# Performance work log

Hardware: AMD Instinct MI355X
Metric: run time of the kernel (lower is better)

## Reference

```python
import jax, jax.numpy as jnp
import numpy as np
from jax import lax

K = 3
STRIDE = 1
PAD = 1


def _active_sites(mask):
    # mask: [B, Cm, H, W] int. A patch is 'active' if ANY element of the
    # unfolded (im2col) patch is nonzero -> max-pool of (mask != 0) over the
    # same kernel/stride/padding window.
    m = jnp.any(mask != 0, axis=1, keepdims=True).astype(jnp.float32)  # [B,1,H,W]
    pooled = lax.reduce_window(
        m, 0.0, lax.max,
        window_dimensions=(1, 1, K, K),
        window_strides=(1, 1, STRIDE, STRIDE),
        padding=((0, 0), (0, 0), (PAD, PAD), (PAD, PAD)))
    return pooled > 0  # [B,1,H_out,W_out] bool


def reference(x, mask, weight, bias):
    # Faithful math of MyConv: conv2d(x, weight) + bias at active patch sites
    # (patches whose mask window contains any nonzero), exact zeros elsewhere.
    # masked_scatter in the original preserves patch order, so this equals
    # active * (conv + bias).
    conv = lax.conv_general_dilated(
        x, weight,
        window_strides=(STRIDE, STRIDE),
        padding=((PAD, PAD), (PAD, PAD)),
        dimension_numbers=('NCHW', 'OIHW', 'NCHW'))  # [B,C_out,H_out,W_out]
    active = _active_sites(mask)
    out = (conv + bias[None, :, None, None]) * active.astype(conv.dtype)
    return out


def setup_inputs() -> dict:
    key = jax.random.key(0)
    k1, k2, k3, k4 = jax.random.split(key, 4)
    B, C_in, C_out, H, W = 8, 128, 128, 128, 128
    x = jax.random.normal(k1, (B, C_in, H, W), dtype=jnp.float32)
    mask = jax.random.randint(k2, (B, 1, H, W), 0, 2, dtype=jnp.int32)
    fan_in = C_in * K * K
    bound = 1.0 / np.sqrt(fan_in)
    weight = jax.random.uniform(k3, (C_out, C_in, K, K), minval=-bound, maxval=bound, dtype=jnp.float32)
    bias = jax.random.uniform(k4, (C_out,), minval=-bound, maxval=bound, dtype=jnp.float32)
    return {"x": x, "mask": mask, "weight": weight, "bias": bias}
```

## Files before the change

kernel.cpp:

```cpp
#include <hip/hip_runtime.h>


typedef __bf16 bf16x8 __attribute__((ext_vector_type(8)));
typedef unsigned short u16x8 __attribute__((ext_vector_type(8)));
typedef float f32x4 __attribute__((ext_vector_type(4)));

__device__ __forceinline__ unsigned short f2bf(float f) {
    unsigned int u = __float_as_uint(f);
    u += 0x7fffu + ((u >> 16) & 1u);
    return (unsigned short)(u >> 16);
}

__global__ void setup_all(const float* __restrict__ x, const float* __restrict__ wgt,
                          unsigned short* __restrict__ xp, unsigned short* __restrict__ wpp) {
    __shared__ float Lf[32 * 132];
    const int t   = threadIdx.x;
    const int bid = blockIdx.x;

    if (bid >= 4160) {
        const int e    = (bid - 4160) * 256 + t;
        const int j    = e & 31;
        const int m    = (e >> 5) & 127;
        const int r    = e >> 12;
        const int kw   = r - (r / 3) * 3;
        const int cbkh = r / 3;
        const int cb   = cbkh & 3;
        const int kh   = cbkh >> 2;
        const int ci   = 4 * (j & 7) + (j >> 3);
        __builtin_nontemporal_store(f2bf(wgt[((m * 128 + cb * 32 + ci) * 3 + kh) * 3 + kw]), &wpp[e]);
        return;
    }

    const int hh2 = bid % 130;
    const int cb  = (bid / 130) & 3;
    const int b   = bid / 520;
    u16x8* slab = (u16x8*)(xp + (size_t)(((b * 4 + cb) * 130 + hh2)) * 4160);
    const u16x8 z = {0, 0, 0, 0, 0, 0, 0, 0};

    if (hh2 == 0 || hh2 == 129) {
        for (int k = t; k < 520; k += 256) __builtin_nontemporal_store(z, &slab[k]);
        return;
    }
    const int h = hh2 - 1;

    #pragma unroll
    for (int u = 0; u < 4; ++u) {
        const int f  = t + 256 * u;
        const int ci = f >> 5;
        const int w4 = f & 31;
        const f32x4 v = __builtin_nontemporal_load(
            (const f32x4*)(x + (((b * 128 + cb * 32 + ci) * 128 + h) << 7) + (w4 << 2)));
        *(f32x4*)&Lf[ci * 132 + (w4 << 2)] = v;
    }
    __syncthreads();

    for (int k = t; k < 520; k += 256) {
        const int r = k >> 2;
        const int c = k & 3;
        u16x8 o;
        if (r == 0 || r == 129) {
            o = z;
        } else {
            const int w  = r - 1;
            const int lc = c ^ ((r + (r >> 2)) & 3);
            #pragma unroll
            for (int s = 0; s < 8; ++s) o[s] = f2bf(Lf[(4 * s + lc) * 132 + w]);
        }
        __builtin_nontemporal_store(o, &slab[k]);
    }
}

__device__ __forceinline__ void stage_slabs(const unsigned char* gx, unsigned char* ls, int t) {
    const int g    = t >> 6;
    const int lane = t & 63;
    #pragma unroll
    for (int u = 0; u < 8; ++u)
        __builtin_amdgcn_global_load_lds(
            (const __attribute__((address_space(1))) unsigned int*)(gx + u * 2048 + g * 1024 + lane * 16),
            (__attribute__((address_space(3))) unsigned int*)(ls + u * 2048 + g * 1024),
            16, 0, 0);
    if (t < 16)
        __builtin_amdgcn_global_load_lds(
            (const __attribute__((address_space(1))) unsigned int*)(gx + 16384 + t * 16),
            (__attribute__((address_space(3))) unsigned int*)(ls + 16384),
            16, 0, 0);
}

__global__ __launch_bounds__(128, 2)
void myconv5(const unsigned short* __restrict__ xp,
             const int* __restrict__ mask,
             const unsigned short* __restrict__ wp,
             const float* __restrict__ bias,
             float* __restrict__ out)
{
    __shared__ __align__(16) unsigned char Xs[2][16640];
    __shared__ float act[256];

    const int t = threadIdx.x;
    const int b     = blockIdx.x & 7;
    const int r8    = blockIdx.x >> 3;
    const int mhalf = r8 & 1;
    const int h0    = (r8 >> 1) << 1;

    const int lane = t & 63;
    const int l16  = lane & 15;
    const int q    = lane >> 4;
    const int g    = t >> 6;

    const unsigned char* xpB = (const unsigned char*)xp;

    stage_slabs(xpB + (size_t)((b * 4 + 0) * 130 + h0 + 0) * 8320, &Xs[0][0], t);

    #pragma unroll
    for (int gg = 0; gg < 2; ++gg) {
        const int h = h0 + gg;
        int any = 0;
        #pragma unroll
        for (int kh = 0; kh < 3; ++kh) {
            int hh = h + kh - 1;
            if ((unsigned)hh < 128u) {
                const int* mrow = mask + (b * 128 + hh) * 128;
                #pragma unroll
                for (int kw = 0; kw < 3; ++kw) {
                    int ww = t + kw - 1;
                    if ((unsigned)ww < 128u) any |= mrow[ww];
                }
            }
        }
        act[gg * 128 + t] = any ? 1.0f : 0.0f;
    }

    int bb[3];
    #pragma unroll
    for (int kw = 0; kw < 3; ++kw) {
        const int rr   = l16 + kw;
        const int slot = q ^ ((rr + (rr >> 2)) & 3);
        bb[kw] = g * 8320 + rr * 64 + (slot << 4);
    }

    const unsigned char* agl = (const unsigned char*)wp + (mhalf * 64 + l16) * 64 + q * 16;

    f32x4 acc[4][8];
    const f32x4 fzero = {0.f, 0.f, 0.f, 0.f};
    #pragma unroll
    for (int i = 0; i < 4; ++i)
        #pragma unroll
        for (int j = 0; j < 8; ++j)
            acc[i][j] = fzero;

    __syncthreads();

    for (int r = 0; r < 12; ++r) {
        if (r < 11) {
            const int rn = r + 1;
            stage_slabs(xpB + (size_t)((b * 4 + (rn & 3)) * 130 + h0 + (rn >> 2)) * 8320,
                        &Xs[(rn & 1)][0], t);
        }

        const unsigned char* ar = agl + r * 24576;
        const unsigned char* xb = &Xs[r & 1][0];
        #pragma unroll
        for (int kw = 0; kw < 3; ++kw) {
            bf16x8 af[4];
            #pragma unroll
            for (int i = 0; i < 4; ++i)
                af[i] = *(const bf16x8*)(ar + kw * 8192 + i * 1024);
            bf16x8 bfr[8];
            #pragma unroll
            for (int j = 0; j < 8; ++j)
                bfr[j] = *(const bf16x8*)(xb + bb[kw] + j * 1024);
            #pragma unroll
            for (int i = 0; i < 4; ++i)
                #pragma unroll
                for (int j = 0; j < 8; ++j)
                    acc[i][j] = __builtin_amdgcn_mfma_f32_16x16x32_bf16(af[i], bfr[j], acc[i][j], 0, 0, 0);
        }

        __syncthreads();
    }

    #pragma unroll
    for (int i = 0; i < 4; ++i) {
        const int m0 = mhalf * 64 + (i << 4) + (q << 2);
        const f32x4 bv = *(const f32x4*)(bias + m0);
        #pragma unroll
        for (int j = 0; j < 8; ++j) {
            const int w = (j << 4) + l16;
            const float a = act[(g << 7) + w];
            float* base = out + (((b << 7) + m0) << 14) + ((h0 + g) << 7) + w;
            #pragma unroll
            for (int rg = 0; rg < 4; ++rg)
                base[rg << 14] = (acc[i][j][rg] + bv[rg]) * a;
        }
    }
}

#define LDAF 40
__global__ __launch_bounds__(256, 2)
void myconv_fb(const float* __restrict__ x,
               const int* __restrict__ mask,
               const float* __restrict__ wgt,
               const float* __restrict__ bias,
               float* __restrict__ out)
{
    __shared__ unsigned short As[128 * LDAF];
    __shared__ unsigned short Bs[128 * LDAF];
    __shared__ float act[128];

    const int t   = threadIdx.x;
    const int blk = blockIdx.x;
    const int b   = blk >> 7;
    const int h   = blk & 127;

    if (t < 128) {
        int any = 0;
        #pragma unroll
        for (int kh = 0; kh < 3; ++kh) {
            int hh = h + kh - 1;
            if ((unsigned)hh < 128u) {
                const int* mrow = mask + (b * 128 + hh) * 128;
                #pragma unroll
                for (int kw = 0; kw < 3; ++kw) {
                    int ww = t + kw - 1;
                    if ((unsigned)ww < 128u) any |= mrow[ww];
                }
            }
        }
        act[t] = any ? 1.0f : 0.0f;
    }

    const int lane = t & 63;
    const int l16  = lane & 15;
    const int half = lane >> 4;
    const int wv   = t >> 6;
    const int wm   = (wv >> 1) << 6;
    const int wn   = (wv & 1) << 6;

    f32x4 acc[4][4];
    const f32x4 fzero = {0.f, 0.f, 0.f, 0.f};
    #pragma unroll
    for (int i = 0; i < 4; ++i)
        #pragma unroll
        for (int j = 0; j < 4; ++j)
            acc[i][j] = fzero;

    const int am  = t >> 3;
    const int ac4 = (t & 7) << 2;
    const int n     = t & 127;
    const int khalf = __builtin_amdgcn_readfirstlane(t >> 7);
    const int xb    = b << 21;

    for (int kt = 0; kt < 36; ++kt) {
        __syncthreads();
        #pragma unroll
        for (int jj = 0; jj < 4; ++jj) {
            const int m = am + (jj << 5);
            const float4 v = *(const float4*)(wgt + m * 1152 + kt * 32 + ac4);
            unsigned short* dst = &As[m * LDAF + ac4];
            dst[0] = f2bf(v.x); dst[1] = f2bf(v.y); dst[2] = f2bf(v.z); dst[3] = f2bf(v.w);
        }
        u16x8 bv0, bv1;
        #pragma unroll
        for (int s = 0; s < 16; ++s) {
            const int k  = kt * 32 + khalf * 16 + s;
            const int ci = (k * 7282) >> 16;
            const int r  = k - ci * 9;
            const int kh = (r >= 3) + (r >= 6);
            const int kw = r - kh * 3;
            const int hh = h + kh - 1;
            float v = 0.f;
            if ((unsigned)hh < 128u) {
                const int ww = n + kw - 1;
                if ((unsigned)ww < 128u)
                    v = x[xb + (ci << 14) + (hh << 7) + ww];
            }
            if (s < 8) bv0[s] = f2bf(v); else bv1[s - 8] = f2bf(v);
        }
        *(u16x8*)&Bs[n * LDAF + khalf * 16]     = bv0;
        *(u16x8*)&Bs[n * LDAF + khalf * 16 + 8] = bv1;

        __syncthreads();

        bf16x8 af[4], bfr[4];
        #pragma unroll
        for (int i = 0; i < 4; ++i)
            af[i] = *(const bf16x8*)&As[(wm + (i << 4) + l16) * LDAF + (half << 3)];
        #pragma unroll
        for (int j = 0; j < 4; ++j)
            bfr[j] = *(const bf16x8*)&Bs[(wn + (j << 4) + l16) * LDAF + (half << 3)];
        #pragma unroll
        for (int i = 0; i < 4; ++i)
            #pragma unroll
            for (int j = 0; j < 4; ++j)
                acc[i][j] = __builtin_amdgcn_mfma_f32_16x16x32_bf16(af[i], bfr[j], acc[i][j], 0, 0, 0);
    }

    #pragma unroll
    for (int i = 0; i < 4; ++i) {
        #pragma unroll
        for (int j = 0; j < 4; ++j) {
            const int ncol = wn + (j << 4) + l16;
            const float a  = act[ncol];
            #pragma unroll
            for (int rg = 0; rg < 4; ++rg) {
                const int m = wm + (i << 4) + (half << 2) + rg;
                out[(((b << 7) + m) << 14) + (h << 7) + ncol] =
                    (acc[i][j][rg] + bias[m]) * a;
            }
        }
    }
}

extern "C" void kernel_launch(void* const* d_in, const int* in_sizes, int n_in,
                              void* d_out, int out_size, void* d_ws, size_t ws_size,
                              hipStream_t stream) {
    const float* x    = (const float*)d_in[0];
    const int*   mask = (const int*)d_in[1];
    const float* wgt  = (const float*)d_in[2];
    const float* bias = (const float*)d_in[3];
    float* out        = (float*)d_out;

    const size_t XP_ELEMS = 4160ull * 4160;
    const size_t WP_ELEMS = 36ull * 128 * 32;
    const size_t need = (XP_ELEMS + WP_ELEMS) * 2;

    if (ws_size >= need) {
        unsigned short* xpw = (unsigned short*)d_ws;
        unsigned short* wpw = xpw + XP_ELEMS;
        setup_all<<<dim3(4736), dim3(256), 0, stream>>>(x, wgt, xpw, wpw);
        myconv5<<<dim3(1024), dim3(128), 0, stream>>>(xpw, mask, wpw, bias, out);
    } else {
        myconv_fb<<<dim3(1024), dim3(256), 0, stream>>>(x, mask, wgt, bias, out);
    }
}
```

Before: 168.8 us.

## Fuse input bf16 conversion into conv staging, drop padded xp prepass

Removes the separate pass that converted x to a padded, swizzled bf16 layout in workspace. The conv kernel now reads fp32 x directly, converts it to bf16 and writes the swizzled rows into LDS itself, zeroing the padding rows inline. This drops a full read-write of the activation tensor through global memory and one kernel launch. In exchange the staging uses strided scalar fp32 loads instead of async global-to-LDS copies, so it no longer overlaps with the MFMA work and each x row is read again by every block that needs it.

```diff
diff --git a/kernel.cpp b/kernel.cpp
--- a/kernel.cpp
+++ b/kernel.cpp
@@ -11,87 +11,49 @@
     return (unsigned short)(u >> 16);
 }
 
-__global__ void setup_all(const float* __restrict__ x, const float* __restrict__ wgt,
-                          unsigned short* __restrict__ xp, unsigned short* __restrict__ wpp) {
-    __shared__ float Lf[32 * 132];
-    const int t   = threadIdx.x;
-    const int bid = blockIdx.x;
-
-    if (bid >= 4160) {
-        const int e    = (bid - 4160) * 256 + t;
-        const int j    = e & 31;
-        const int m    = (e >> 5) & 127;
-        const int r    = e >> 12;
-        const int kw   = r - (r / 3) * 3;
-        const int cbkh = r / 3;
-        const int cb   = cbkh & 3;
-        const int kh   = cbkh >> 2;
-        const int ci   = 4 * (j & 7) + (j >> 3);
-        __builtin_nontemporal_store(f2bf(wgt[((m * 128 + cb * 32 + ci) * 3 + kh) * 3 + kw]), &wpp[e]);
-        return;
-    }
-
-    const int hh2 = bid % 130;
-    const int cb  = (bid / 130) & 3;
-    const int b   = bid / 520;
-    u16x8* slab = (u16x8*)(xp + (size_t)(((b * 4 + cb) * 130 + hh2)) * 4160);
-    const u16x8 z = {0, 0, 0, 0, 0, 0, 0, 0};
-
-    if (hh2 == 0 || hh2 == 129) {
-        for (int k = t; k < 520; k += 256) __builtin_nontemporal_store(z, &slab[k]);
-        return;
-    }
-    const int h = hh2 - 1;
-
-    #pragma unroll
-    for (int u = 0; u < 4; ++u) {
-        const int f  = t + 256 * u;
-        const int ci = f >> 5;
-        const int w4 = f & 31;
-        const f32x4 v = __builtin_nontemporal_load(
-            (const f32x4*)(x + (((b * 128 + cb * 32 + ci) * 128 + h) << 7) + (w4 << 2)));
-        *(f32x4*)&Lf[ci * 132 + (w4 << 2)] = v;
-    }
-    __syncthreads();
-
-    for (int k = t; k < 520; k += 256) {
-        const int r = k >> 2;
-        const int c = k & 3;
-        u16x8 o;
-        if (r == 0 || r == 129) {
-            o = z;
-        } else {
-            const int w  = r - 1;
-            const int lc = c ^ ((r + (r >> 2)) & 3);
-            #pragma unroll
-            for (int s = 0; s < 8; ++s) o[s] = f2bf(Lf[(4 * s + lc) * 132 + w]);
-        }
-        __builtin_nontemporal_store(o, &slab[k]);
-    }
-}
-
-__device__ __forceinline__ void stage_slabs(const unsigned char* gx, unsigned char* ls, int t) {
-    const int g    = t >> 6;
-    const int lane = t & 63;
-    #pragma unroll
-    for (int u = 0; u < 8; ++u)
-        __builtin_amdgcn_global_load_lds(
-            (const __attribute__((address_space(1))) unsigned int*)(gx + u * 2048 + g * 1024 + lane * 16),
-            (__attribute__((address_space(3))) unsigned int*)(ls + u * 2048 + g * 1024),
-            16, 0, 0);
-    if (t < 16)
-        __builtin_amdgcn_global_load_lds(
-            (const __attribute__((address_space(1))) unsigned int*)(gx + 16384 + t * 16),
-            (__attribute__((address_space(3))) unsigned int*)(ls + 16384),
-            16, 0, 0);
+__global__ void setup_wp(const float* __restrict__ wgt, unsigned short* __restrict__ wpp) {
+    const int e    = blockIdx.x * 256 + threadIdx.x;
+    const int j    = e & 31;
+    const int m    = (e >> 5) & 127;
+    const int r    = e >> 12;
+    const int kw   = r - (r / 3) * 3;
+    const int cbkh = r / 3;
+    const int cb   = cbkh & 3;
+    const int kh   = cbkh >> 2;
+    const int ci   = 4 * (j & 7) + (j >> 3);
+    wpp[e] = f2bf(wgt[((m * 128 + cb * 32 + ci) * 3 + kh) * 3 + kw]);
+}
+
+__device__ __forceinline__ void stage_conv(const float* __restrict__ x,
+                                           unsigned char* XsN,
+                                           int b, int cb, int hb, int t) {
+    const u16x8 z  = {0, 0, 0, 0, 0, 0, 0, 0};
+    const int rr   = t + 1;
+    const int cswz = (rr + (rr >> 2)) & 3;
+    #pragma unroll
+    for (int y = 0; y < 2; ++y) {
+        const int h    = hb + y;
+        const bool inb = (unsigned)h < 128u;
+        const float* xr = x + ((((b * 128 + cb * 32) * 128) + h) << 7) + t;
+        #pragma unroll
+        for (int lc = 0; lc < 4; ++lc) {
+            u16x8 o = z;
+            if (inb) {
+                #pragma unroll
+                for (int s = 0; s < 8; ++s)
+                    o[s] = f2bf(xr[(lc << 14) + (s << 16)]);
+            }
+            *(u16x8*)(XsN + y * 8320 + rr * 64 + ((lc ^ cswz) << 4)) = o;
+        }
+    }
 }
 
 __global__ __launch_bounds__(128, 2)
-void myconv5(const unsigned short* __restrict__ xp,
-             const int* __restrict__ mask,
-             const unsigned short* __restrict__ wp,
-             const float* __restrict__ bias,
-             float* __restrict__ out)
+void myconv11(const float* __restrict__ x,
+              const int* __restrict__ mask,
+              const unsigned short* __restrict__ wp,
+              const float* __restrict__ bias,
+              float* __restrict__ out)
 {
     __shared__ __align__(16) unsigned char Xs[2][16640];
     __shared__ float act[256];
@@ -107,9 +69,16 @@
     const int q    = lane >> 4;
     const int g    = t >> 6;
 
-    const unsigned char* xpB = (const unsigned char*)xp;
-
-    stage_slabs(xpB + (size_t)((b * 4 + 0) * 130 + h0 + 0) * 8320, &Xs[0][0], t);
+    if (t < 32) {
+        const u16x8 z = {0, 0, 0, 0, 0, 0, 0, 0};
+        const int bf = (t >> 4) & 1;
+        const int y  = (t >> 3) & 1;
+        const int rr = ((t >> 2) & 1) ? 129 : 0;
+        const int c  = t & 3;
+        *(u16x8*)(&Xs[bf][0] + y * 8320 + rr * 64 + (c << 4)) = z;
+    }
+
+    stage_conv(x, &Xs[0][0], b, 0, h0 - 1, t);
 
     #pragma unroll
     for (int gg = 0; gg < 2; ++gg) {
@@ -153,8 +122,7 @@
     for (int r = 0; r < 12; ++r) {
         if (r < 11) {
             const int rn = r + 1;
-            stage_slabs(xpB + (size_t)((b * 4 + (rn & 3)) * 130 + h0 + (rn >> 2)) * 8320,
-                        &Xs[(rn & 1)][0], t);
+            stage_conv(x, &Xs[rn & 1][0], b, rn & 3, h0 + (rn >> 2) - 1, t);
         }
 
         const unsigned char* ar = agl + r * 24576;
@@ -320,15 +288,11 @@
     const float* bias = (const float*)d_in[3];
     float* out        = (float*)d_out;
 
-    const size_t XP_ELEMS = 4160ull * 4160;
     const size_t WP_ELEMS = 36ull * 128 * 32;
-    const size_t need = (XP_ELEMS + WP_ELEMS) * 2;
-
-    if (ws_size >= need) {
-        unsigned short* xpw = (unsigned short*)d_ws;
-        unsigned short* wpw = xpw + XP_ELEMS;
-        setup_all<<<dim3(4736), dim3(256), 0, stream>>>(x, wgt, xpw, wpw);
-        myconv5<<<dim3(1024), dim3(128), 0, stream>>>(xpw, mask, wpw, bias, out);
+    if (ws_size >= WP_ELEMS * 2) {
+        unsigned short* wpw = (unsigned short*)d_ws;
+        setup_wp<<<dim3(576), dim3(256), 0, stream>>>(wgt, wpw);
+        myconv11<<<dim3(1024), dim3(128), 0, stream>>>(x, mask, wpw, bias, out);
     } else {
         myconv_fb<<<dim3(1024), dim3(256), 0, stream>>>(x, mask, wgt, bias, out);
     }
```

After: 162.6 us. -3.6%, faster.
